# Optimization experiments

Measured on AMD Instinct MI355X. Metric: run time of the kernel, lower is better.

## Reference

```python
import jax, jax.numpy as jnp
import numpy as np

N_NODES = 100000
N_EDGES = 300000
D = 256
EPS = 1e-5
ALPHA = 0.5  # residual_alpha


def setup_inputs() -> dict:
    key = jax.random.key(0)
    ks = jax.random.split(key, 6)
    x = jax.random.normal(ks[0], (N_NODES, D), dtype=jnp.float32)
    edge_index = jax.random.randint(ks[1], (2, N_EDGES), 0, N_NODES, dtype=jnp.int32)
    edge_weight = jax.random.uniform(ks[2], (N_EDGES,), dtype=jnp.float32)
    # GCNConv parameters (glorot-ish weight, bias)
    W = jax.random.normal(ks[3], (D, D), dtype=jnp.float32) / np.float32(np.sqrt(D))
    b = 0.01 * jax.random.normal(ks[4], (D,), dtype=jnp.float32)
    # LayerNorm parameters
    gamma = jnp.ones((D,), dtype=jnp.float32)
    beta = jnp.zeros((D,), dtype=jnp.float32)
    return {"x": x, "edge_index": edge_index, "edge_weight": edge_weight,
            "W": W, "b": b, "gamma": gamma, "beta": beta}


def gcn_residual(x, edge_index, edge_weight, W, b, gamma, beta):
    src, dst = edge_index[0], edge_index[1]
    # linear transform first (PyG GCNConv order)
    h = x @ W  # [N, D]
    # gcn_norm with added self-loops (self-loop weight = 1)
    deg = jax.ops.segment_sum(edge_weight, dst, num_segments=N_NODES) + 1.0  # [N]
    dinv = jax.lax.rsqrt(deg)
    norm = dinv[src] * edge_weight * dinv[dst]  # [E]
    # message + aggregate (scatter-add over destination nodes)
    agg = jax.ops.segment_sum(norm[:, None] * h[src], dst, num_segments=N_NODES)
    agg = agg + (dinv * dinv)[:, None] * h  # self-loop contribution
    h = agg + b
    # LayerNorm over feature dim
    mu = jnp.mean(h, axis=-1, keepdims=True)
    var = jnp.mean(jnp.square(h - mu), axis=-1, keepdims=True)
    h = (h - mu) * jax.lax.rsqrt(var + EPS) * gamma + beta
    # dropout p=0.0 -> identity; weighted residual; relu
    h = ALPHA * h + (1.0 - ALPHA) * x
    return jax.nn.relu(h)


def reference(x, edge_index, edge_weight, W, b, gamma, beta):
    return gcn_residual(x, edge_index, edge_weight, W, b, gamma, beta)
```

## Files before the change

### kernel.cpp

```cpp
#include <hip/hip_runtime.h>


#define NN 100000
#define NE 300000
#define DD 256
#define NB 391
#define GMB 1563

typedef __attribute__((ext_vector_type(8))) short short8;
typedef __attribute__((ext_vector_type(4))) short short4v;
typedef __attribute__((ext_vector_type(4))) float f32x4;
typedef __attribute__((ext_vector_type(4))) unsigned short u16x4;

static __device__ __forceinline__ short f2bf(float f) {
  union { float f; unsigned u; } a; a.f = f;
  unsigned r = a.u + 0x7fffu + ((a.u >> 16) & 1u);
  return (short)(r >> 16);
}

static __device__ __forceinline__ float bf2f(short s) {
  return __uint_as_float((unsigned)(unsigned short)s << 16);
}

__global__ __launch_bounds__(256) void k_init(float* __restrict__ dv,
                                              int* __restrict__ cnt) {
  int i = blockIdx.x * 256 + threadIdx.x;
  if (i < NN) { dv[i] = 0.0f; cnt[i] = 0; }
}

__global__ __launch_bounds__(256) void k_hist(const int* __restrict__ ei,
                                              const float* __restrict__ ew,
                                              float* __restrict__ dv,
                                              int* __restrict__ cnt) {
  int e = blockIdx.x * 256 + threadIdx.x;
  if (e < NE) {
    int d = ei[NE + e];
    atomicAdd(&dv[d], ew[e]);
    atomicAdd(&cnt[d], 1);
  }
}

__global__ __launch_bounds__(256) void k_dinv(float* __restrict__ dv) {
  int i = blockIdx.x * 256 + threadIdx.x;
  if (i < NN) dv[i] = rsqrtf(dv[i] + 1.0f);
}

__global__ __launch_bounds__(256) void k_scan1(const int* __restrict__ cnt,
                                               int* __restrict__ off,
                                               int* __restrict__ bsum) {
  __shared__ int tmp[256];
  int t = threadIdx.x;
  int i = blockIdx.x * 256 + t;
  int v = (i < NN) ? cnt[i] : 0;
  tmp[t] = v;
  __syncthreads();
  for (int o = 1; o < 256; o <<= 1) {
    int u = (t >= o) ? tmp[t - o] : 0;
    __syncthreads();
    tmp[t] += u;
    __syncthreads();
  }
  if (i < NN) off[i] = tmp[t] - v;
  if (t == 255) bsum[blockIdx.x] = tmp[t];
}

__global__ __launch_bounds__(512) void k_scan2(int* __restrict__ bsum) {
  __shared__ int tmp[512];
  int t = threadIdx.x;
  int v = (t < NB) ? bsum[t] : 0;
  tmp[t] = v;
  __syncthreads();
  for (int o = 1; o < 512; o <<= 1) {
    int u = (t >= o) ? tmp[t - o] : 0;
    __syncthreads();
    tmp[t] += u;
    __syncthreads();
  }
  bsum[t] = tmp[t] - v;
}

__global__ __launch_bounds__(256) void k_scan3(int* __restrict__ off,
                                               const int* __restrict__ bsum,
                                               int* __restrict__ cur) {
  int i = blockIdx.x * 256 + threadIdx.x;
  if (i < NN) {
    int o = off[i] + bsum[i >> 8];
    off[i] = o;
    cur[i] = o;
  }
}

__global__ __launch_bounds__(256) void k_place(const int* __restrict__ ei,
                                               const float* __restrict__ ew,
                                               const float* __restrict__ dv,
                                               int* __restrict__ cur,
                                               int2* __restrict__ elist) {
  int e = blockIdx.x * 256 + threadIdx.x;
  if (e >= NE) return;
  int s = ei[e];
  int d = ei[NE + e];
  float c = dv[s] * ew[e] * dv[d];
  int pos = atomicAdd(&cur[d], 1);
  elist[pos] = make_int2(s, __float_as_int(c));
}

__global__ __launch_bounds__(256) void k_wprep(const float* __restrict__ W,
                                               short* __restrict__ Wf) {
  int idx = blockIdx.x * 256 + threadIdx.x;
  int k = idx >> 6;
  int c4 = idx & 63;
  const float4 v = *(const float4*)(W + k * 256 + c4 * 4);
  float vv[4] = {v.x, v.y, v.z, v.w};
#pragma unroll
  for (int i = 0; i < 4; ++i) {
    int c = c4 * 4 + i;
    int di = ((k >> 5) * 16 + (c >> 4)) * 512 + ((c & 15) + ((k >> 3) & 3) * 16) * 8 + (k & 7);
    Wf[di] = f2bf(vv[i]);
  }
}

__global__ __launch_bounds__(512) void k_gemm(const float* __restrict__ x,
                                              const short* __restrict__ Wf,
                                              short* __restrict__ h) {
  __shared__ short As[64 * 256];

  const int t = threadIdx.x;
  const int lane = t & 63;
  const int wid = t >> 6;
  const int row0 = blockIdx.x * 64;
  const int wrow = (wid >> 2) * 32;
  const int wstrip = (wid & 3);

  float4 va[4], vb[4];
#pragma unroll
  for (int i = 0; i < 4; ++i) {
    int p = i * 512 + t;
    int r = p >> 5;
    int kp = p & 31;
    int grow = row0 + r;
    if (grow < NN) {
      const float* src = x + (size_t)grow * 256 + kp * 8;
      va[i] = *(const float4*)(src);
      vb[i] = *(const float4*)(src + 4);
    } else {
      va[i] = make_float4(0.f, 0.f, 0.f, 0.f);
      vb[i] = va[i];
    }
  }
#pragma unroll
  for (int i = 0; i < 4; ++i) {
    int p = i * 512 + t;
    int r = p >> 5;
    int kp = p & 31;
    short8 s;
    s[0] = f2bf(va[i].x); s[1] = f2bf(va[i].y); s[2] = f2bf(va[i].z); s[3] = f2bf(va[i].w);
    s[4] = f2bf(vb[i].x); s[5] = f2bf(vb[i].y); s[6] = f2bf(vb[i].z); s[7] = f2bf(vb[i].w);
    int byte = (r * 512 + kp * 16) ^ ((r & 7) << 4);
    *(short8*)((char*)As + byte) = s;
  }
  __syncthreads();

  f32x4 acc[4][2];
#pragma unroll
  for (int mc = 0; mc < 4; ++mc)
#pragma unroll
    for (int nr = 0; nr < 2; ++nr) acc[mc][nr] = (f32x4)0.0f;

  const short* wbase = Wf + (size_t)(wstrip * 4) * 512 + lane * 8;

#pragma unroll
  for (int ks = 0; ks < 8; ++ks) {
    short8 bx[2];
    short8 aw[4];
#pragma unroll
    for (int nr = 0; nr < 2; ++nr) {
      int r = wrow + nr * 16 + (lane & 15);
      int byte = (r * 512 + ks * 64 + (lane >> 4) * 16) ^ ((r & 7) << 4);
      bx[nr] = *(short8*)((char*)As + byte);
    }
#pragma unroll
    for (int mc = 0; mc < 4; ++mc)
      aw[mc] = *(const short8*)(wbase + (size_t)(ks * 16 + mc) * 512);
#pragma unroll
    for (int mc = 0; mc < 4; ++mc)
#pragma unroll
      for (int nr = 0; nr < 2; ++nr)
        acc[mc][nr] = __builtin_amdgcn_mfma_f32_16x16x32_bf16(
            aw[mc], bx[nr], acc[mc][nr], 0, 0, 0);
  }

#pragma unroll
  for (int mc = 0; mc < 4; ++mc) {
    int cbase = wstrip * 64 + mc * 16 + 4 * (lane >> 4);
#pragma unroll
    for (int nr = 0; nr < 2; ++nr) {
      int r = row0 + wrow + nr * 16 + (lane & 15);
      if (r < NN) {
        u16x4 s;
        s[0] = (unsigned short)f2bf(acc[mc][nr][0]);
        s[1] = (unsigned short)f2bf(acc[mc][nr][1]);
        s[2] = (unsigned short)f2bf(acc[mc][nr][2]);
        s[3] = (unsigned short)f2bf(acc[mc][nr][3]);
        *(u16x4*)(h + (size_t)r * 256 + cbase) = s;
      }
    }
  }
}

__global__ __launch_bounds__(256) void k_agg(const short* __restrict__ h,
                                             const float* __restrict__ dv,
                                             const int* __restrict__ cnt,
                                             const int* __restrict__ off,
                                             const int2* __restrict__ elist,
                                             const float* __restrict__ x,
                                             const float* __restrict__ b,
                                             const float* __restrict__ gamma,
                                             const float* __restrict__ beta,
                                             float* __restrict__ out) {
  int node = (blockIdx.x * 256 + threadIdx.x) >> 5;
  if (node >= NN) return;
  int q = threadIdx.x & 31;

  const float di = dv[node];
  const float d2 = di * di;
  short8 hv = *(const short8*)(h + (size_t)node * 256 + q * 8);
  float a[8];
#pragma unroll
  for (int i = 0; i < 8; ++i) a[i] = bf2f(hv[i]) * d2;

  const int n = cnt[node];
  const int st = off[node];
  int j = 0;
  for (; j + 2 <= n; j += 2) {
    int2 r0 = elist[st + j];
    int2 r1 = elist[st + j + 1];
    short8 g0 = *(const short8*)(h + (size_t)r0.x * 256 + q * 8);
    short8 g1 = *(const short8*)(h + (size_t)r1.x * 256 + q * 8);
    float c0 = __int_as_float(r0.y);
    float c1 = __int_as_float(r1.y);
#pragma unroll
    for (int i = 0; i < 8; ++i) a[i] += c0 * bf2f(g0[i]);
#pragma unroll
    for (int i = 0; i < 8; ++i) a[i] += c1 * bf2f(g1[i]);
  }
  if (j < n) {
    int2 r0 = elist[st + j];
    short8 g0 = *(const short8*)(h + (size_t)r0.x * 256 + q * 8);
    float c0 = __int_as_float(r0.y);
#pragma unroll
    for (int i = 0; i < 8; ++i) a[i] += c0 * bf2f(g0[i]);
  }

  const float4 b0 = *(const float4*)(b + q * 8);
  const float4 b1 = *(const float4*)(b + q * 8 + 4);
  a[0] += b0.x; a[1] += b0.y; a[2] += b0.z; a[3] += b0.w;
  a[4] += b1.x; a[5] += b1.y; a[6] += b1.z; a[7] += b1.w;

  float s = 0.f, ss = 0.f;
#pragma unroll
  for (int i = 0; i < 8; ++i) { s += a[i]; ss += a[i] * a[i]; }
#pragma unroll
  for (int o = 16; o > 0; o >>= 1) {
    s += __shfl_xor(s, o);
    ss += __shfl_xor(ss, o);
  }
  const float mu = s * (1.0f / 256.0f);
  const float var = ss * (1.0f / 256.0f) - mu * mu;
  const float inv = rsqrtf(var + 1e-5f);

  const float4 g0 = *(const float4*)(gamma + q * 8);
  const float4 g1 = *(const float4*)(gamma + q * 8 + 4);
  const float4 e0 = *(const float4*)(beta + q * 8);
  const float4 e1 = *(const float4*)(beta + q * 8 + 4);
  const float4 x0 = *(const float4*)(x + (size_t)node * 256 + q * 8);
  const float4 x1 = *(const float4*)(x + (size_t)node * 256 + q * 8 + 4);

  float4 r0, r1;
  r0.x = fmaxf(0.5f * ((a[0] - mu) * inv * g0.x + e0.x) + 0.5f * x0.x, 0.f);
  r0.y = fmaxf(0.5f * ((a[1] - mu) * inv * g0.y + e0.y) + 0.5f * x0.y, 0.f);
  r0.z = fmaxf(0.5f * ((a[2] - mu) * inv * g0.z + e0.z) + 0.5f * x0.z, 0.f);
  r0.w = fmaxf(0.5f * ((a[3] - mu) * inv * g0.w + e0.w) + 0.5f * x0.w, 0.f);
  r1.x = fmaxf(0.5f * ((a[4] - mu) * inv * g1.x + e1.x) + 0.5f * x1.x, 0.f);
  r1.y = fmaxf(0.5f * ((a[5] - mu) * inv * g1.y + e1.y) + 0.5f * x1.y, 0.f);
  r1.z = fmaxf(0.5f * ((a[6] - mu) * inv * g1.z + e1.z) + 0.5f * x1.z, 0.f);
  r1.w = fmaxf(0.5f * ((a[7] - mu) * inv * g1.w + e1.w) + 0.5f * x1.w, 0.f);

  float* o = out + (size_t)node * 256 + q * 8;
  *(float4*)(o) = r0;
  *(float4*)(o + 4) = r1;
}

extern "C" void kernel_launch(void* const* d_in, const int* in_sizes, int n_in,
                              void* d_out, int out_size, void* d_ws, size_t ws_size,
                              hipStream_t stream) {
  const float* x     = (const float*)d_in[0];
  const int*   ei    = (const int*)d_in[1];
  const float* ew    = (const float*)d_in[2];
  const float* W     = (const float*)d_in[3];
  const float* b     = (const float*)d_in[4];
  const float* gamma = (const float*)d_in[5];
  const float* beta  = (const float*)d_in[6];
  float* out = (float*)d_out;

  short* h   = (short*)d_ws;
  float* dv  = (float*)(h + (size_t)NN * DD);
  int*   cnt = (int*)(dv + NN);
  int*   off = cnt + NN;
  int*   cur = off + NN;
  int*   bsum = cur + NN;
  int2*  elist = (int2*)(bsum + 512);
  short* Wf  = (short*)(elist + NE);

  k_init<<<NB, 256, 0, stream>>>(dv, cnt);
  k_hist<<<(NE + 255) / 256, 256, 0, stream>>>(ei, ew, dv, cnt);
  k_dinv<<<NB, 256, 0, stream>>>(dv);
  k_scan1<<<NB, 256, 0, stream>>>(cnt, off, bsum);
  k_scan2<<<1, 512, 0, stream>>>(bsum);
  k_scan3<<<NB, 256, 0, stream>>>(off, bsum, cur);
  k_place<<<(NE + 255) / 256, 256, 0, stream>>>(ei, ew, dv, cur, elist);

  k_wprep<<<64, 256, 0, stream>>>(W, Wf);
  k_gemm<<<GMB, 512, 0, stream>>>(x, Wf, h);

  k_agg<<<(NN * 32 + 255) / 256, 256, 0, stream>>>(h, dv, cnt, off, elist, x, b, gamma, beta, out);
}
```

Before: 172.7 us.

## Pipeline GEMM A-tile staging by K-chunks and unroll gather loop by four

The GEMM kernel now loads all x rows up front, then writes LDS in four K-chunks, each followed by a lightweight barrier and the MFMAs for that chunk. MFMA work can start before the whole tile is staged. Out-of-range rows are clamped instead of zero-filled, and launch bounds request two blocks per CU. The aggregation loop processes four neighbors per iteration to raise memory-level parallelism, at the cost of higher register pressure.

```diff
diff --git a/kernel.cpp b/kernel.cpp
--- a/kernel.cpp
+++ b/kernel.cpp
@@ -8,7 +8,6 @@
 #define GMB 1563
 
 typedef __attribute__((ext_vector_type(8))) short short8;
-typedef __attribute__((ext_vector_type(4))) short short4v;
 typedef __attribute__((ext_vector_type(4))) float f32x4;
 typedef __attribute__((ext_vector_type(4))) unsigned short u16x4;
 
@@ -119,9 +118,9 @@
   }
 }
 
-__global__ __launch_bounds__(512) void k_gemm(const float* __restrict__ x,
-                                              const short* __restrict__ Wf,
-                                              short* __restrict__ h) {
+__global__ __launch_bounds__(512, 2) void k_gemm(const float* __restrict__ x,
+                                                 const short* __restrict__ Wf,
+                                                 short* __restrict__ h) {
   __shared__ short As[64 * 256];
 
   const int t = threadIdx.x;
@@ -129,36 +128,32 @@
   const int wid = t >> 6;
   const int row0 = blockIdx.x * 64;
   const int wrow = (wid >> 2) * 32;
-  const int wstrip = (wid & 3);
-
-  float4 va[4], vb[4];
-#pragma unroll
-  for (int i = 0; i < 4; ++i) {
-    int p = i * 512 + t;
-    int r = p >> 5;
-    int kp = p & 31;
-    int grow = row0 + r;
-    if (grow < NN) {
-      const float* src = x + (size_t)grow * 256 + kp * 8;
-      va[i] = *(const float4*)(src);
-      vb[i] = *(const float4*)(src + 4);
-    } else {
-      va[i] = make_float4(0.f, 0.f, 0.f, 0.f);
-      vb[i] = va[i];
-    }
-  }
-#pragma unroll
-  for (int i = 0; i < 4; ++i) {
-    int p = i * 512 + t;
-    int r = p >> 5;
-    int kp = p & 31;
-    short8 s;
-    s[0] = f2bf(va[i].x); s[1] = f2bf(va[i].y); s[2] = f2bf(va[i].z); s[3] = f2bf(va[i].w);
-    s[4] = f2bf(vb[i].x); s[5] = f2bf(vb[i].y); s[6] = f2bf(vb[i].z); s[7] = f2bf(vb[i].w);
-    int byte = (r * 512 + kp * 16) ^ ((r & 7) << 4);
-    *(short8*)((char*)As + byte) = s;
-  }
-  __syncthreads();
+  const int wstrip = wid & 3;
+
+  const int rr = t >> 3;
+  const int kc = t & 7;
+  int grow = row0 + rr;
+  if (grow > NN - 1) grow = NN - 1;
+  const float* rp = x + (size_t)grow * 256 + kc * 8;
+  float4 a0 = *(const float4*)(rp);        float4 b0 = *(const float4*)(rp + 4);
+  float4 a1 = *(const float4*)(rp + 64);   float4 b1 = *(const float4*)(rp + 68);
+  float4 a2 = *(const float4*)(rp + 128);  float4 b2 = *(const float4*)(rp + 132);
+  float4 a3 = *(const float4*)(rp + 192);  float4 b3 = *(const float4*)(rp + 196);
+
+  const int wb = (rr * 512 + kc * 16) ^ ((rr & 7) << 4);
+
+#define WRITE_REGION(I, A, B)                                              \
+  {                                                                        \
+    short8 s_;                                                             \
+    s_[0] = f2bf(A.x); s_[1] = f2bf(A.y); s_[2] = f2bf(A.z);               \
+    s_[3] = f2bf(A.w); s_[4] = f2bf(B.x); s_[5] = f2bf(B.y);               \
+    s_[6] = f2bf(B.z); s_[7] = f2bf(B.w);                                  \
+    *(short8*)((char*)As + wb + (I)*128) = s_;                             \
+  }
+
+#define BARSYNC                                                            \
+  asm volatile("s_waitcnt lgkmcnt(0)" ::: "memory");                       \
+  __builtin_amdgcn_s_barrier();
 
   f32x4 acc[4][2];
 #pragma unroll
@@ -168,26 +163,45 @@
 
   const short* wbase = Wf + (size_t)(wstrip * 4) * 512 + lane * 8;
 
-#pragma unroll
-  for (int ks = 0; ks < 8; ++ks) {
-    short8 bx[2];
-    short8 aw[4];
-#pragma unroll
-    for (int nr = 0; nr < 2; ++nr) {
-      int r = wrow + nr * 16 + (lane & 15);
-      int byte = (r * 512 + ks * 64 + (lane >> 4) * 16) ^ ((r & 7) << 4);
-      bx[nr] = *(short8*)((char*)As + byte);
-    }
-#pragma unroll
-    for (int mc = 0; mc < 4; ++mc)
-      aw[mc] = *(const short8*)(wbase + (size_t)(ks * 16 + mc) * 512);
-#pragma unroll
-    for (int mc = 0; mc < 4; ++mc)
-#pragma unroll
-      for (int nr = 0; nr < 2; ++nr)
-        acc[mc][nr] = __builtin_amdgcn_mfma_f32_16x16x32_bf16(
-            aw[mc], bx[nr], acc[mc][nr], 0, 0, 0);
-  }
+#define COMPUTE_REGION(I)                                                  \
+  _Pragma("unroll")                                                        \
+  for (int ks2 = 0; ks2 < 2; ++ks2) {                                      \
+    const int ks = 2 * (I) + ks2;                                          \
+    short8 bx[2];                                                          \
+    short8 aw[4];                                                          \
+    _Pragma("unroll")                                                      \
+    for (int nr = 0; nr < 2; ++nr) {                                       \
+      int r_ = wrow + nr * 16 + (lane & 15);                               \
+      int byte_ = (r_ * 512 + ks * 64 + (lane >> 4) * 16) ^ ((r_ & 7) << 4); \
+      bx[nr] = *(short8*)((char*)As + byte_);                              \
+    }                                                                      \
+    _Pragma("unroll")                                                      \
+    for (int mc = 0; mc < 4; ++mc)                                         \
+      aw[mc] = *(const short8*)(wbase + (size_t)(ks * 16 + mc) * 512);     \
+    _Pragma("unroll")                                                      \
+    for (int mc = 0; mc < 4; ++mc)                                         \
+      _Pragma("unroll")                                                    \
+      for (int nr = 0; nr < 2; ++nr)                                       \
+        acc[mc][nr] = __builtin_amdgcn_mfma_f32_16x16x32_bf16(             \
+            aw[mc], bx[nr], acc[mc][nr], 0, 0, 0);                         \
+  }
+
+  WRITE_REGION(0, a0, b0);
+  BARSYNC;
+  COMPUTE_REGION(0);
+  WRITE_REGION(1, a1, b1);
+  BARSYNC;
+  COMPUTE_REGION(1);
+  WRITE_REGION(2, a2, b2);
+  BARSYNC;
+  COMPUTE_REGION(2);
+  WRITE_REGION(3, a3, b3);
+  BARSYNC;
+  COMPUTE_REGION(3);
+
+#undef WRITE_REGION
+#undef BARSYNC
+#undef COMPUTE_REGION
 
 #pragma unroll
   for (int mc = 0; mc < 4; ++mc) {
@@ -231,19 +245,24 @@
   const int n = cnt[node];
   const int st = off[node];
   int j = 0;
-  for (; j + 2 <= n; j += 2) {
+  for (; j + 4 <= n; j += 4) {
     int2 r0 = elist[st + j];
     int2 r1 = elist[st + j + 1];
+    int2 r2 = elist[st + j + 2];
+    int2 r3 = elist[st + j + 3];
     short8 g0 = *(const short8*)(h + (size_t)r0.x * 256 + q * 8);
     short8 g1 = *(const short8*)(h + (size_t)r1.x * 256 + q * 8);
+    short8 g2 = *(const short8*)(h + (size_t)r2.x * 256 + q * 8);
+    short8 g3 = *(const short8*)(h + (size_t)r3.x * 256 + q * 8);
     float c0 = __int_as_float(r0.y);
     float c1 = __int_as_float(r1.y);
-#pragma unroll
-    for (int i = 0; i < 8; ++i) a[i] += c0 * bf2f(g0[i]);
-#pragma unroll
-    for (int i = 0; i < 8; ++i) a[i] += c1 * bf2f(g1[i]);
-  }
-  if (j < n) {
+    float c2 = __int_as_float(r2.y);
+    float c3 = __int_as_float(r3.y);
+#pragma unroll
+    for (int i = 0; i < 8; ++i)
+      a[i] += c0 * bf2f(g0[i]) + c1 * bf2f(g1[i]) + c2 * bf2f(g2[i]) + c3 * bf2f(g3[i]);
+  }
+  for (; j < n; ++j) {
     int2 r0 = elist[st + j];
     short8 g0 = *(const short8*)(h + (size_t)r0.x * 256 + q * 8);
     float c0 = __int_as_float(r0.y);
```

Result: faster. 164.8 us (-4.6%).

## Drop LDS staging in GEMM, load x directly into MFMA fragments; unroll gather by 4

Applied to the files above, without the earlier changes.

The GEMM kernel no longer stages a 64-row bf16 tile of x in shared memory. Each 256-thread block now handles 16 rows, with each lane loading its own x fragment straight from global memory and converting it to bf16 in registers, and four waves splitting the output columns. This removes the LDS round trip and the barrier, but each x row is loaded by four waves and there are four times as many blocks. The aggregation loop is also unrolled to four edges per iteration, putting more gathers in flight.

```diff
diff --git a/kernel.cpp b/kernel.cpp
--- a/kernel.cpp
+++ b/kernel.cpp
@@ -5,10 +5,9 @@
 #define NE 300000
 #define DD 256
 #define NB 391
-#define GMB 1563
+#define GMB 6250
 
 typedef __attribute__((ext_vector_type(8))) short short8;
-typedef __attribute__((ext_vector_type(4))) short short4v;
 typedef __attribute__((ext_vector_type(4))) float f32x4;
 typedef __attribute__((ext_vector_type(4))) unsigned short u16x4;
 
@@ -119,90 +118,57 @@
   }
 }
 
-__global__ __launch_bounds__(512) void k_gemm(const float* __restrict__ x,
+__global__ __launch_bounds__(256) void k_gemm(const float* __restrict__ x,
                                               const short* __restrict__ Wf,
                                               short* __restrict__ h) {
-  __shared__ short As[64 * 256];
-
   const int t = threadIdx.x;
   const int lane = t & 63;
-  const int wid = t >> 6;
-  const int row0 = blockIdx.x * 64;
-  const int wrow = (wid >> 2) * 32;
-  const int wstrip = (wid & 3);
-
-  float4 va[4], vb[4];
-#pragma unroll
-  for (int i = 0; i < 4; ++i) {
-    int p = i * 512 + t;
-    int r = p >> 5;
-    int kp = p & 31;
-    int grow = row0 + r;
-    if (grow < NN) {
-      const float* src = x + (size_t)grow * 256 + kp * 8;
-      va[i] = *(const float4*)(src);
-      vb[i] = *(const float4*)(src + 4);
-    } else {
-      va[i] = make_float4(0.f, 0.f, 0.f, 0.f);
-      vb[i] = va[i];
-    }
-  }
-#pragma unroll
-  for (int i = 0; i < 4; ++i) {
-    int p = i * 512 + t;
-    int r = p >> 5;
-    int kp = p & 31;
-    short8 s;
-    s[0] = f2bf(va[i].x); s[1] = f2bf(va[i].y); s[2] = f2bf(va[i].z); s[3] = f2bf(va[i].w);
-    s[4] = f2bf(vb[i].x); s[5] = f2bf(vb[i].y); s[6] = f2bf(vb[i].z); s[7] = f2bf(vb[i].w);
-    int byte = (r * 512 + kp * 16) ^ ((r & 7) << 4);
-    *(short8*)((char*)As + byte) = s;
-  }
-  __syncthreads();
-
-  f32x4 acc[4][2];
-#pragma unroll
-  for (int mc = 0; mc < 4; ++mc)
-#pragma unroll
-    for (int nr = 0; nr < 2; ++nr) acc[mc][nr] = (f32x4)0.0f;
+  const int wstrip = t >> 6;
+  const int row0 = blockIdx.x * 16;
+
+  int r = row0 + (lane & 15);
+  int rc = (r < NN) ? r : (NN - 1);
+  const float* rp = x + (size_t)rc * 256 + (lane >> 4) * 8;
+
+  float4 fa[8], fb[8];
+#pragma unroll
+  for (int ks = 0; ks < 8; ++ks) {
+    fa[ks] = *(const float4*)(rp + ks * 32);
+    fb[ks] = *(const float4*)(rp + ks * 32 + 4);
+  }
+
+  f32x4 acc[4];
+#pragma unroll
+  for (int mc = 0; mc < 4; ++mc) acc[mc] = (f32x4)0.0f;
 
   const short* wbase = Wf + (size_t)(wstrip * 4) * 512 + lane * 8;
 
 #pragma unroll
   for (int ks = 0; ks < 8; ++ks) {
-    short8 bx[2];
+    short8 bx;
+    bx[0] = f2bf(fa[ks].x); bx[1] = f2bf(fa[ks].y);
+    bx[2] = f2bf(fa[ks].z); bx[3] = f2bf(fa[ks].w);
+    bx[4] = f2bf(fb[ks].x); bx[5] = f2bf(fb[ks].y);
+    bx[6] = f2bf(fb[ks].z); bx[7] = f2bf(fb[ks].w);
     short8 aw[4];
-#pragma unroll
-    for (int nr = 0; nr < 2; ++nr) {
-      int r = wrow + nr * 16 + (lane & 15);
-      int byte = (r * 512 + ks * 64 + (lane >> 4) * 16) ^ ((r & 7) << 4);
-      bx[nr] = *(short8*)((char*)As + byte);
-    }
 #pragma unroll
     for (int mc = 0; mc < 4; ++mc)
       aw[mc] = *(const short8*)(wbase + (size_t)(ks * 16 + mc) * 512);
 #pragma unroll
     for (int mc = 0; mc < 4; ++mc)
-#pragma unroll
-      for (int nr = 0; nr < 2; ++nr)
-        acc[mc][nr] = __builtin_amdgcn_mfma_f32_16x16x32_bf16(
-            aw[mc], bx[nr], acc[mc][nr], 0, 0, 0);
-  }
-
-#pragma unroll
-  for (int mc = 0; mc < 4; ++mc) {
-    int cbase = wstrip * 64 + mc * 16 + 4 * (lane >> 4);
-#pragma unroll
-    for (int nr = 0; nr < 2; ++nr) {
-      int r = row0 + wrow + nr * 16 + (lane & 15);
-      if (r < NN) {
-        u16x4 s;
-        s[0] = (unsigned short)f2bf(acc[mc][nr][0]);
-        s[1] = (unsigned short)f2bf(acc[mc][nr][1]);
-        s[2] = (unsigned short)f2bf(acc[mc][nr][2]);
-        s[3] = (unsigned short)f2bf(acc[mc][nr][3]);
-        *(u16x4*)(h + (size_t)r * 256 + cbase) = s;
-      }
+      acc[mc] = __builtin_amdgcn_mfma_f32_16x16x32_bf16(aw[mc], bx, acc[mc], 0, 0, 0);
+  }
+
+  if (r < NN) {
+#pragma unroll
+    for (int mc = 0; mc < 4; ++mc) {
+      int cbase = wstrip * 64 + mc * 16 + 4 * (lane >> 4);
+      u16x4 s;
+      s[0] = (unsigned short)f2bf(acc[mc][0]);
+      s[1] = (unsigned short)f2bf(acc[mc][1]);
+      s[2] = (unsigned short)f2bf(acc[mc][2]);
+      s[3] = (unsigned short)f2bf(acc[mc][3]);
+      *(u16x4*)(h + (size_t)r * 256 + cbase) = s;
     }
   }
 }
@@ -231,19 +197,24 @@
   const int n = cnt[node];
   const int st = off[node];
   int j = 0;
-  for (; j + 2 <= n; j += 2) {
+  for (; j + 4 <= n; j += 4) {
     int2 r0 = elist[st + j];
     int2 r1 = elist[st + j + 1];
+    int2 r2 = elist[st + j + 2];
+    int2 r3 = elist[st + j + 3];
     short8 g0 = *(const short8*)(h + (size_t)r0.x * 256 + q * 8);
     short8 g1 = *(const short8*)(h + (size_t)r1.x * 256 + q * 8);
+    short8 g2 = *(const short8*)(h + (size_t)r2.x * 256 + q * 8);
+    short8 g3 = *(const short8*)(h + (size_t)r3.x * 256 + q * 8);
     float c0 = __int_as_float(r0.y);
     float c1 = __int_as_float(r1.y);
-#pragma unroll
-    for (int i = 0; i < 8; ++i) a[i] += c0 * bf2f(g0[i]);
-#pragma unroll
-    for (int i = 0; i < 8; ++i) a[i] += c1 * bf2f(g1[i]);
-  }
-  if (j < n) {
+    float c2 = __int_as_float(r2.y);
+    float c3 = __int_as_float(r3.y);
+#pragma unroll
+    for (int i = 0; i < 8; ++i)
+      a[i] += c0 * bf2f(g0[i]) + c1 * bf2f(g1[i]) + c2 * bf2f(g2[i]) + c3 * bf2f(g3[i]);
+  }
+  for (; j < n; ++j) {
     int2 r0 = elist[st + j];
     short8 g0 = *(const short8*)(h + (size_t)r0.x * 256 + q * 8);
     float c0 = __int_as_float(r0.y);
@@ -320,7 +291,7 @@
   k_place<<<(NE + 255) / 256, 256, 0, stream>>>(ei, ew, dv, cur, elist);
 
   k_wprep<<<64, 256, 0, stream>>>(W, Wf);
-  k_gemm<<<GMB, 512, 0, stream>>>(x, Wf, h);
+  k_gemm<<<GMB, 256, 0, stream>>>(x, Wf, h);
 
   k_agg<<<(NN * 32 + 255) / 256, 256, 0, stream>>>(h, dv, cnt, off, elist, x, b, gamma, beta, out);
 }
```

Measured after the change: 200.9 us. 16.3% more time.
